# Optimization experiments

Measured on AMD Instinct MI355X. Metric: run time of the kernel, lower is better.

The kernel has to match this reference:

```python
import jax, jax.numpy as jnp
import numpy as np

IN_F = 256
OUT_F = 256
ALPHA = 0.01  # LeakyReLU negative slope
NEG_INF = -1e9


def setup_inputs() -> dict:
    key = jax.random.key(0)
    k_inp, k_adj, k_W, k_a = jax.random.split(key, 4)
    inp = jax.random.normal(k_inp, (8, 2048, IN_F), dtype=jnp.float32)
    adj = jax.random.randint(k_adj, (2048, 2048), 0, 2, dtype=jnp.int32)
    # xavier_uniform with gain=1.414
    gain = 1.414
    lim_W = gain * np.sqrt(6.0 / (IN_F + OUT_F))
    W = jax.random.uniform(k_W, (IN_F, OUT_F), minval=-lim_W, maxval=lim_W, dtype=jnp.float32)
    lim_a = gain * np.sqrt(6.0 / (2 * OUT_F + 1))
    a = jax.random.uniform(k_a, (2 * OUT_F, 1), minval=-lim_a, maxval=lim_a, dtype=jnp.float32)
    return {"inp": inp, "adj": adj, "W": W, "a": a}


def reference(inp, adj, W, a):
    # h: [B, N, F]
    h = jnp.matmul(inp, W)
    # Additive attention decomposed: e_ij = leaky_relu(h_i . a1 + h_j . a2)
    # (mathematically identical to concat([h_i, h_j]) @ a, without the O(N^2 * 2F) intermediate)
    a1 = a[:OUT_F, 0]  # [F]
    a2 = a[OUT_F:, 0]  # [F]
    e_src = jnp.einsum('bnf,f->bn', h, a1)  # [B, N]
    e_dst = jnp.einsum('bnf,f->bn', h, a2)  # [B, N]
    e = jax.nn.leaky_relu(e_src[:, :, None] + e_dst[:, None, :], negative_slope=ALPHA)  # [B, N, N]
    e = jnp.where(adj[None, :, :] == 0, NEG_INF, e)
    attention = jax.nn.softmax(e, axis=-1)
    # dropout is identity in eval mode
    h_prime = jnp.matmul(attention, h)  # [B, N, F]
    return jax.nn.relu(h_prime)  # concat=True path
```

## Files before the change

### kernel.cpp

```cpp
#include <hip/hip_runtime.h>
#include <hip/hip_bf16.h>
#include <stdint.h>

#define N_NODES 2048
#define FDIM 256

typedef short bf16x8 __attribute__((ext_vector_type(8)));
typedef float f32x4 __attribute__((ext_vector_type(4)));
typedef unsigned short u16x4 __attribute__((ext_vector_type(4)));

static __device__ __forceinline__ unsigned short bf16r(float x) {
  __hip_bfloat16 h = __float2bfloat16(x);
  return __builtin_bit_cast(unsigned short, h);
}

static __device__ __forceinline__ void gl_lds16(const void* g, void* l) {
  __builtin_amdgcn_global_load_lds(
      (const __attribute__((address_space(1))) unsigned int*)g,
      (__attribute__((address_space(3))) unsigned int*)l, 16, 0, 0);
}

__global__ __launch_bounds__(256) void k_prep(const float* __restrict__ W, const float* __restrict__ a,
                                              __hip_bfloat16* __restrict__ WT16,
                                              float* __restrict__ wa1, float* __restrict__ wa2) {
  int bid = blockIdx.x, t = threadIdx.x;
  if (bid < 16) {
    __shared__ __hip_bfloat16 T[64][67];
    int k0 = (bid & 3) * 64, f0 = (bid >> 2) * 64;
    int r = t >> 2, c0 = (t & 3) * 16;
    #pragma unroll
    for (int i = 0; i < 4; ++i) {
      f32x4 v = *(const f32x4*)(W + (size_t)(k0 + r) * FDIM + f0 + c0 + i * 4);
      #pragma unroll
      for (int j = 0; j < 4; ++j) T[r][c0 + i * 4 + j] = __float2bfloat16(v[j]);
    }
    __syncthreads();
    int fr = t >> 2, kc = (t & 3) * 16;
    unsigned short buf[16];
    #pragma unroll
    for (int i = 0; i < 16; ++i) buf[i] = __builtin_bit_cast(unsigned short, T[kc + i][fr]);
    uint4* dst = (uint4*)(WT16 + (size_t)(f0 + fr) * FDIM + k0 + kc);
    dst[0] = *(uint4*)&buf[0];
    dst[1] = *(uint4*)&buf[8];
  } else {
    int k = (bid - 16) * 64 + (t >> 2), q = t & 3;
    float s1 = 0.f, s2 = 0.f;
    #pragma unroll
    for (int i = 0; i < 16; ++i) {
      int f = q * 64 + i * 4;
      f32x4 w  = *(const f32x4*)(W + (size_t)k * FDIM + f);
      f32x4 v1 = *(const f32x4*)(a + f);
      f32x4 v2 = *(const f32x4*)(a + FDIM + f);
      #pragma unroll
      for (int j = 0; j < 4; ++j) { s1 += w[j] * v1[j]; s2 += w[j] * v2[j]; }
    }
    s1 += __shfl_xor(s1, 1); s1 += __shfl_xor(s1, 2);
    s2 += __shfl_xor(s2, 1); s2 += __shfl_xor(s2, 2);
    if (q == 0) { wa1[k] = s1; wa2[k] = s2; }
  }
}

__global__ __launch_bounds__(256) void k_h(const float* __restrict__ inp,
                                           const __hip_bfloat16* __restrict__ WT16,
                                           const float* __restrict__ wa1, const float* __restrict__ wa2,
                                           __hip_bfloat16* __restrict__ hT,
                                           float* __restrict__ e_src, float* __restrict__ e_dst) {
  __shared__ char lds_raw[20480];
  __hip_bfloat16* Asm = (__hip_bfloat16*)lds_raw;
  int t = threadIdx.x;
  int r0 = blockIdx.x * 32;
  int b = r0 >> 11, j0 = r0 & (N_NODES - 1);
  {
    int r = t >> 3, q = t & 7, c0 = q * 32;
    const float* ip = inp + (size_t)(r0 + r) * FDIM + c0;
    float s1 = 0.f, s2 = 0.f;
    #pragma unroll
    for (int i = 0; i < 8; ++i) {
      f32x4 v  = *(const f32x4*)(ip + i * 4);
      f32x4 u1 = *(const f32x4*)(wa1 + c0 + i * 4);
      f32x4 u2 = *(const f32x4*)(wa2 + c0 + i * 4);
      u16x4 pk;
      #pragma unroll
      for (int j = 0; j < 4; ++j) {
        s1 += v[j] * u1[j];
        s2 += v[j] * u2[j];
        pk[j] = bf16r(v[j]);
      }
      *(u16x4*)(Asm + r * 264 + c0 + i * 4) = pk;
    }
    s1 += __shfl_xor(s1, 1); s1 += __shfl_xor(s1, 2); s1 += __shfl_xor(s1, 4);
    s2 += __shfl_xor(s2, 1); s2 += __shfl_xor(s2, 2); s2 += __shfl_xor(s2, 4);
    if (q == 0) { e_src[r0 + r] = s1; e_dst[r0 + r] = s2; }
  }
  __syncthreads();

  int lane = t & 63, wv = t >> 6, l15 = lane & 15, lq = lane >> 4;
  int f0 = wv * 64;
  f32x4 acc[2][4];
  #pragma unroll
  for (int mf = 0; mf < 2; ++mf)
    #pragma unroll
    for (int nf = 0; nf < 4; ++nf)
      #pragma unroll
      for (int e = 0; e < 4; ++e) acc[mf][nf][e] = 0.f;

  #pragma unroll
  for (int ks = 0; ks < 8; ++ks) {
    int k0 = ks * 32;
    bf16x8 af[2], bfr[4];
    #pragma unroll
    for (int mf = 0; mf < 2; ++mf)
      af[mf] = *(const bf16x8*)(Asm + (mf * 16 + l15) * 264 + k0 + lq * 8);
    #pragma unroll
    for (int nf = 0; nf < 4; ++nf)
      bfr[nf] = *(const bf16x8*)(WT16 + (size_t)(f0 + nf * 16 + l15) * FDIM + k0 + lq * 8);
    #pragma unroll
    for (int mf = 0; mf < 2; ++mf)
      #pragma unroll
      for (int nf = 0; nf < 4; ++nf)
        acc[mf][nf] = __builtin_amdgcn_mfma_f32_16x16x32_bf16(af[mf], bfr[nf], acc[mf][nf], 0, 0, 0);
  }

  __syncthreads();
  __hip_bfloat16* Tsm = (__hip_bfloat16*)lds_raw;
  #pragma unroll
  for (int mf = 0; mf < 2; ++mf)
    #pragma unroll
    for (int nf = 0; nf < 4; ++nf) {
      u16x4 pk;
      #pragma unroll
      for (int r = 0; r < 4; ++r) pk[r] = bf16r(acc[mf][nf][r]);
      int fl = f0 + nf * 16 + l15;
      int jl = mf * 16 + lq * 4;
      *(u16x4*)(Tsm + fl * 40 + jl) = pk;
    }
  __syncthreads();
  {
    const uint4* src = (const uint4*)(Tsm + t * 40);
    uint4* dst = (uint4*)(hT + ((size_t)b * FDIM + t) * N_NODES + j0);
    dst[0] = src[0]; dst[1] = src[1]; dst[2] = src[2]; dst[3] = src[3];
  }
}

__global__ __launch_bounds__(512) void k_mlp(const int* __restrict__ adj,
                                             const float* __restrict__ e_src,
                                             const float* __restrict__ e_dst,
                                             __hip_bfloat16* __restrict__ P) {
  int t = threadIdx.x, i = blockIdx.x;
  int b = t >> 6, l = t & 63;
  float es = e_src[(b << 11) + i];
  const float* edb = e_dst + ((size_t)b << 11);
  const int* arow = adj + (size_t)i * N_NODES;
  float ev[8][4];
  float mx = -3e38f;
  #pragma unroll
  for (int it = 0; it < 8; ++it) {
    int j0 = it * 256 + l * 4;
    int4 av  = *(const int4*)(arow + j0);
    f32x4 ed = *(const f32x4*)(edb + j0);
    const int* avp = (const int*)&av;
    #pragma unroll
    for (int c = 0; c < 4; ++c) {
      float s = es + ed[c];
      float lr = fmaxf(s, 0.01f * s);
      float e = (avp[c] != 0) ? lr : -1e9f;
      ev[it][c] = e;
      mx = fmaxf(mx, e);
    }
  }
  #pragma unroll
  for (int m = 1; m <= 32; m <<= 1) mx = fmaxf(mx, __shfl_xor(mx, m));
  float sum = 0.f;
  #pragma unroll
  for (int it = 0; it < 8; ++it)
    #pragma unroll
    for (int c = 0; c < 4; ++c) {
      ev[it][c] = __expf(ev[it][c] - mx);
      sum += ev[it][c];
    }
  #pragma unroll
  for (int m = 1; m <= 32; m <<= 1) sum += __shfl_xor(sum, m);
  float il = 1.0f / sum;
  __hip_bfloat16* Pr = P + (((size_t)b << 11) + i) * N_NODES;
  #pragma unroll
  for (int it = 0; it < 8; ++it) {
    int j0 = it * 256 + l * 4;
    u16x4 pk;
    #pragma unroll
    for (int c = 0; c < 4; ++c) pk[c] = bf16r(ev[it][c] * il);
    *(u16x4*)(Pr + j0) = pk;
  }
}

__global__ __launch_bounds__(512) void k_pv(const __hip_bfloat16* __restrict__ P,
                                            const __hip_bfloat16* __restrict__ hT,
                                            float* __restrict__ out) {
  __shared__ __hip_bfloat16 Asm[2 * 64 * 64];
  __shared__ __hip_bfloat16 Bsm[2 * 256 * 64];
  int t = threadIdx.x;
  int b = blockIdx.x & 7;
  int i0 = (blockIdx.x >> 3) * 64;
  int lane = t & 63, wv = t >> 6, l15 = lane & 15, lq = lane >> 4;
  int wm = wv >> 1, wn = wv & 1;
  const __hip_bfloat16* Ab  = P  + ((size_t)(b << 11) + i0) * N_NODES;
  const __hip_bfloat16* hTb = hT + (size_t)b * FDIM * N_NODES;

  int sr = t >> 3, sc = t & 7;
  auto stage = [&](int buf, int js) {
    {
      int cs = sc ^ (sr & 7);
      gl_lds16(Ab + (size_t)sr * N_NODES + js + cs * 8, Asm + buf * 4096 + wv * 512);
    }
    #pragma unroll
    for (int p = 0; p < 4; ++p) {
      int r = p * 64 + sr;
      int cs = sc ^ (r & 7);
      gl_lds16(hTb + (size_t)r * N_NODES + js + cs * 8, Bsm + buf * 16384 + p * 4096 + wv * 512);
    }
  };

  f32x4 acc[8];
  #pragma unroll
  for (int nf = 0; nf < 8; ++nf)
    #pragma unroll
    for (int e = 0; e < 4; ++e) acc[nf][e] = 0.f;

  stage(0, 0);
  __syncthreads();

  int arow = wm * 16 + l15;
  for (int ks = 0; ks < 32; ++ks) {
    int cur = ks & 1;
    if (ks != 31) stage(cur ^ 1, (ks + 1) * 64);
    const __hip_bfloat16* Al = Asm + cur * 4096;
    const __hip_bfloat16* Bl = Bsm + cur * 16384;
    #pragma unroll
    for (int ko = 0; ko < 2; ++ko) {
      int g = ko * 4 + lq;
      bf16x8 af = *(const bf16x8*)(Al + arow * 64 + (g ^ (arow & 7)) * 8);
      #pragma unroll
      for (int nf = 0; nf < 8; ++nf) {
        int br = wn * 128 + nf * 16 + l15;
        bf16x8 bfr = *(const bf16x8*)(Bl + br * 64 + (g ^ (br & 7)) * 8);
        acc[nf] = __builtin_amdgcn_mfma_f32_16x16x32_bf16(af, bfr, acc[nf], 0, 0, 0);
      }
    }
    __syncthreads();
  }

  #pragma unroll
  for (int nf = 0; nf < 8; ++nf)
    #pragma unroll
    for (int r = 0; r < 4; ++r) {
      int row = i0 + wm * 16 + lq * 4 + r;
      int col = wn * 128 + nf * 16 + l15;
      out[((size_t)(b << 11) + row) * FDIM + col] = fmaxf(acc[nf][r], 0.0f);
    }
}

__global__ __launch_bounds__(256) void k_pack(const int* __restrict__ adj, uint32_t* __restrict__ adjp) {
  int t = threadIdx.x;
  int lane = t & 63;
  int i = blockIdx.x * 4 + (t >> 6);
  const int* row = adj + (size_t)i * N_NODES;
  #pragma unroll
  for (int it = 0; it < 32; ++it) {
    int v = row[it * 64 + lane];
    unsigned long long m = __ballot(v != 0);
    if (lane == 0) {
      adjp[i * 64 + it * 2]     = (uint32_t)(m & 0xffffffffull);
      adjp[i * 64 + it * 2 + 1] = (uint32_t)(m >> 32);
    }
  }
}

__global__ __launch_bounds__(256) void k_ml(const uint32_t* __restrict__ adjp,
                                            const float* __restrict__ e_src,
                                            const float* __restrict__ e_dst,
                                            float* __restrict__ mrow, float* __restrict__ ilrow) {
  int t = threadIdx.x;
  int lane = t & 63;
  int r = blockIdx.x * 4 + (t >> 6);
  int b = r >> 11, i = r & (N_NODES - 1);
  float es = e_src[r];
  const float* edb = e_dst + ((size_t)b << 11);
  const uint32_t* arow = adjp + (size_t)i * 64;
  float ev[32];
  float mx = -3e38f;
  #pragma unroll
  for (int it = 0; it < 32; ++it) {
    int j = it * 64 + lane;
    float ed = edb[j];
    uint32_t w = arow[j >> 5];
    float s = es + ed;
    float lr = fmaxf(s, 0.01f * s);
    float e = ((w >> (j & 31)) & 1u) ? lr : -1e9f;
    ev[it] = e;
    mx = fmaxf(mx, e);
  }
  #pragma unroll
  for (int m = 1; m <= 32; m <<= 1) mx = fmaxf(mx, __shfl_xor(mx, m));
  float sum = 0.f;
  #pragma unroll
  for (int it = 0; it < 32; ++it) sum += __expf(ev[it] - mx);
  #pragma unroll
  for (int m = 1; m <= 32; m <<= 1) sum += __shfl_xor(sum, m);
  if (lane == 0) { mrow[r] = mx; ilrow[r] = 1.0f / sum; }
}

__global__ __launch_bounds__(256) void k_pv_f(const __hip_bfloat16* __restrict__ hT,
                                              const uint32_t* __restrict__ adjp,
                                              const float* __restrict__ e_src,
                                              const float* __restrict__ e_dst,
                                              const float* __restrict__ mrow,
                                              const float* __restrict__ ilrow,
                                              float* __restrict__ out) {
  __shared__ __hip_bfloat16 Psm[2][64 * 40];
  int t = threadIdx.x;
  int bb = blockIdx.x & 7;
  int i0 = ((blockIdx.x >> 3) & 31) * 64;
  int fh = (blockIdx.x >> 8) * 128;
  int ip = t >> 2, jq = t & 3;
  int rflat = (bb << 11) + i0 + ip;
  float es = e_src[rflat], mi = mrow[rflat], ili = ilrow[rflat];
  const uint32_t* arow = adjp + (size_t)(i0 + ip) * 64;
  const float* edb = e_dst + ((size_t)bb << 11);
  const __hip_bfloat16* hTb = hT + (size_t)bb * FDIM * N_NODES;
  int lane = t & 63, wv = t >> 6, l15 = lane & 15, lq = lane >> 4;
  int wm = wv >> 1, wn = wv & 1;
  const __hip_bfloat16* bp[4];
  #pragma unroll
  for (int nf = 0; nf < 4; ++nf)
    bp[nf] = hTb + (size_t)(fh + wn * 64 + nf * 16 + l15) * N_NODES + lq * 8;

  auto computeP = [&](int js) -> uint4 {
    uint32_t word = arow[js >> 5] >> (jq * 8);
    f32x4 e0 = *(const f32x4*)(edb + js + jq * 8);
    f32x4 e1 = *(const f32x4*)(edb + js + jq * 8 + 4);
    unsigned short u[8];
    #pragma unroll
    for (int d = 0; d < 8; ++d) {
      float edv = (d < 4) ? e0[d] : e1[d & 3];
      float s = es + edv;
      float lr = fmaxf(s, 0.01f * s);
      float e = ((word >> d) & 1u) ? lr : -1e9f;
      u[d] = bf16r(__expf(e - mi) * ili);
    }
    uint4 r;
    r.x = (uint32_t)u[0] | ((uint32_t)u[1] << 16);
    r.y = (uint32_t)u[2] | ((uint32_t)u[3] << 16);
    r.z = (uint32_t)u[4] | ((uint32_t)u[5] << 16);
    r.w = (uint32_t)u[6] | ((uint32_t)u[7] << 16);
    return r;
  };

  f32x4 acc[2][4];
  #pragma unroll
  for (int mf = 0; mf < 2; ++mf)
    #pragma unroll
    for (int nf = 0; nf < 4; ++nf)
      #pragma unroll
      for (int e = 0; e < 4; ++e) acc[mf][nf][e] = 0.f;

  {
    uint4 p0 = computeP(0);
    *(uint4*)((char*)Psm[0] + ip * 80 + jq * 16) = p0;
  }
  bf16x8 bcur[4];
  #pragma unroll
  for (int nf = 0; nf < 4; ++nf) bcur[nf] = *(const bf16x8*)(bp[nf]);
  __syncthreads();

  int cur = 0;
  for (int js = 0; js < N_NODES; js += 32) {
    bf16x8 bn[4];
    bool more = (js + 32) < N_NODES;
    if (more) {
      #pragma unroll
      for (int nf = 0; nf < 4; ++nf) bn[nf] = *(const bf16x8*)(bp[nf] + js + 32);
      uint4 pn = computeP(js + 32);
      *(uint4*)((char*)Psm[cur ^ 1] + ip * 80 + jq * 16) = pn;
    }
    bf16x8 af[2];
    #pragma unroll
    for (int mf = 0; mf < 2; ++mf)
      af[mf] = *(const bf16x8*)((char*)Psm[cur] + (wm * 32 + mf * 16 + l15) * 80 + lq * 16);
    #pragma unroll
    for (int mf = 0; mf < 2; ++mf)
      #pragma unroll
      for (int nf = 0; nf < 4; ++nf)
        acc[mf][nf] = __builtin_amdgcn_mfma_f32_16x16x32_bf16(af[mf], bcur[nf], acc[mf][nf], 0, 0, 0);
    __syncthreads();
    if (more) {
      #pragma unroll
      for (int nf = 0; nf < 4; ++nf) bcur[nf] = bn[nf];
    }
    cur ^= 1;
  }

  #pragma unroll
  for (int mf = 0; mf < 2; ++mf)
    #pragma unroll
    for (int nf = 0; nf < 4; ++nf)
      #pragma unroll
      for (int r = 0; r < 4; ++r) {
        int row = i0 + wm * 32 + mf * 16 + lq * 4 + r;
        int col = fh + wn * 64 + nf * 16 + l15;
        out[((size_t)bb * N_NODES + row) * FDIM + col] = fmaxf(acc[mf][nf][r], 0.0f);
      }
}

extern "C" void kernel_launch(void* const* d_in, const int* in_sizes, int n_in,
                              void* d_out, int out_size, void* d_ws, size_t ws_size,
                              hipStream_t stream) {
  const float* inp = (const float*)d_in[0];
  const int*   adj = (const int*)d_in[1];
  const float* W   = (const float*)d_in[2];
  const float* a   = (const float*)d_in[3];
  float* out = (float*)d_out;
  char* ws = (char*)d_ws;

  const size_t NEED_BIG = 75761664ull;
  if (ws_size >= NEED_BIG) {
    __hip_bfloat16* P    = (__hip_bfloat16*)ws;
    __hip_bfloat16* hT   = (__hip_bfloat16*)(ws + 67108864);
    float* e_src         = (float*)(ws + 75497472);
    float* e_dst         = (float*)(ws + 75563008);
    __hip_bfloat16* WT16 = (__hip_bfloat16*)(ws + 75628544);
    float* wa1           = (float*)(ws + 75759616);
    float* wa2           = (float*)(ws + 75760640);

    k_prep<<<20, 256, 0, stream>>>(W, a, WT16, wa1, wa2);
    k_h<<<512, 256, 0, stream>>>(inp, WT16, wa1, wa2, hT, e_src, e_dst);
    k_mlp<<<2048, 512, 0, stream>>>(adj, e_src, e_dst, P);
    k_pv<<<256, 512, 0, stream>>>(P, hT, out);
  } else {
    __hip_bfloat16* hT   = (__hip_bfloat16*)ws;
    uint32_t* adjp       = (uint32_t*)(ws + 8388608);
    float* e_src         = (float*)(ws + 8912896);
    float* e_dst         = (float*)(ws + 8978432);
    float* mrow          = (float*)(ws + 9043968);
    float* ilrow         = (float*)(ws + 9109504);
    __hip_bfloat16* WT16 = (__hip_bfloat16*)(ws + 9175040);
    float* wa1           = (float*)(ws + 9306112);
    float* wa2           = (float*)(ws + 9307136);

    k_pack<<<512, 256, 0, stream>>>(adj, adjp);
    k_prep<<<20, 256, 0, stream>>>(W, a, WT16, wa1, wa2);
    k_h<<<512, 256, 0, stream>>>(inp, WT16, wa1, wa2, hT, e_src, e_dst);
    k_ml<<<4096, 256, 0, stream>>>(adjp, e_src, e_dst, mrow, ilrow);
    k_pv_f<<<512, 256, 0, stream>>>(hT, adjp, e_src, e_dst, mrow, ilrow, out);
  }
}
```

Measured before the change: 92.74 us.

## Store P and h in MFMA fragment order and drop LDS staging in PV GEMM

The h-producing and softmax kernels now write their bf16 outputs pre-swizzled into the per-lane MFMA fragment layout. This lets the PV GEMM load fragments directly from global memory with coalesced 16-byte loads and register double-buffering, with no LDS staging and no barriers. The PV wave tiling changes from 4x2 to 2x4 with 2x4 fragment accumulators. The trade-off is that reuse now comes from L2 instead of LDS, and the stores in the softmax kernel are scattered across fragment tiles.

New measurement: 113.8 us, median of 5. +22.7%, slower.

```diff
diff --git a/kernel.cpp b/kernel.cpp
--- a/kernel.cpp
+++ b/kernel.cpp
@@ -12,12 +12,6 @@
 static __device__ __forceinline__ unsigned short bf16r(float x) {
   __hip_bfloat16 h = __float2bfloat16(x);
   return __builtin_bit_cast(unsigned short, h);
-}
-
-static __device__ __forceinline__ void gl_lds16(const void* g, void* l) {
-  __builtin_amdgcn_global_load_lds(
-      (const __attribute__((address_space(1))) unsigned int*)g,
-      (__attribute__((address_space(3))) unsigned int*)l, 16, 0, 0);
 }
 
 __global__ __launch_bounds__(256) void k_prep(const float* __restrict__ W, const float* __restrict__ a,
@@ -58,6 +52,224 @@
     s2 += __shfl_xor(s2, 1); s2 += __shfl_xor(s2, 2);
     if (q == 0) { wa1[k] = s1; wa2[k] = s2; }
   }
+}
+
+__global__ __launch_bounds__(256) void k_h2(const float* __restrict__ inp,
+                                            const __hip_bfloat16* __restrict__ WT16,
+                                            const float* __restrict__ wa1, const float* __restrict__ wa2,
+                                            __hip_bfloat16* __restrict__ Bf,
+                                            float* __restrict__ e_src, float* __restrict__ e_dst) {
+  __shared__ char lds_raw[20480];
+  __hip_bfloat16* Asm = (__hip_bfloat16*)lds_raw;
+  int t = threadIdx.x;
+  int r0 = blockIdx.x * 32;
+  int b = r0 >> 11, j0 = r0 & (N_NODES - 1);
+  {
+    int r = t >> 3, q = t & 7, c0 = q * 32;
+    const float* ip = inp + (size_t)(r0 + r) * FDIM + c0;
+    float s1 = 0.f, s2 = 0.f;
+    #pragma unroll
+    for (int i = 0; i < 8; ++i) {
+      f32x4 v  = *(const f32x4*)(ip + i * 4);
+      f32x4 u1 = *(const f32x4*)(wa1 + c0 + i * 4);
+      f32x4 u2 = *(const f32x4*)(wa2 + c0 + i * 4);
+      u16x4 pk;
+      #pragma unroll
+      for (int j = 0; j < 4; ++j) {
+        s1 += v[j] * u1[j];
+        s2 += v[j] * u2[j];
+        pk[j] = bf16r(v[j]);
+      }
+      *(u16x4*)(Asm + r * 264 + c0 + i * 4) = pk;
+    }
+    s1 += __shfl_xor(s1, 1); s1 += __shfl_xor(s1, 2); s1 += __shfl_xor(s1, 4);
+    s2 += __shfl_xor(s2, 1); s2 += __shfl_xor(s2, 2); s2 += __shfl_xor(s2, 4);
+    if (q == 0) { e_src[r0 + r] = s1; e_dst[r0 + r] = s2; }
+  }
+  __syncthreads();
+
+  int lane = t & 63, wv = t >> 6, l15 = lane & 15, lq = lane >> 4;
+  int f0 = wv * 64;
+  f32x4 acc[2][4];
+  #pragma unroll
+  for (int mf = 0; mf < 2; ++mf)
+    #pragma unroll
+    for (int nf = 0; nf < 4; ++nf)
+      #pragma unroll
+      for (int e = 0; e < 4; ++e) acc[mf][nf][e] = 0.f;
+
+  #pragma unroll
+  for (int ks = 0; ks < 8; ++ks) {
+    int k0 = ks * 32;
+    bf16x8 af[2], bfr[4];
+    #pragma unroll
+    for (int mf = 0; mf < 2; ++mf)
+      af[mf] = *(const bf16x8*)(Asm + (mf * 16 + l15) * 264 + k0 + lq * 8);
+    #pragma unroll
+    for (int nf = 0; nf < 4; ++nf)
+      bfr[nf] = *(const bf16x8*)(WT16 + (size_t)(f0 + nf * 16 + l15) * FDIM + k0 + lq * 8);
+    #pragma unroll
+    for (int mf = 0; mf < 2; ++mf)
+      #pragma unroll
+      for (int nf = 0; nf < 4; ++nf)
+        acc[mf][nf] = __builtin_amdgcn_mfma_f32_16x16x32_bf16(af[mf], bfr[nf], acc[mf][nf], 0, 0, 0);
+  }
+
+  __syncthreads();
+  __hip_bfloat16* Tsm = (__hip_bfloat16*)lds_raw;
+  #pragma unroll
+  for (int mf = 0; mf < 2; ++mf)
+    #pragma unroll
+    for (int nf = 0; nf < 4; ++nf) {
+      u16x4 pk;
+      #pragma unroll
+      for (int r = 0; r < 4; ++r) pk[r] = bf16r(acc[mf][nf][r]);
+      int fl = f0 + nf * 16 + l15;
+      int jl = mf * 16 + lq * 4;
+      *(u16x4*)(Tsm + fl * 40 + jl) = pk;
+    }
+  __syncthreads();
+  {
+    int kt = j0 >> 5;
+    #pragma unroll
+    for (int q = 0; q < 4; ++q) {
+      int ft = (t >> 6) * 4 + q;
+      uint4 v = *(const uint4*)(Tsm + (ft * 16 + l15) * 40 + lq * 8);
+      *(uint4*)(Bf + ((((size_t)b * 16 + ft) * 64 + kt) * 64 + lane) * 8) = v;
+    }
+  }
+}
+
+__global__ __launch_bounds__(512) void k_mlp(const int* __restrict__ adj,
+                                             const float* __restrict__ e_src,
+                                             const float* __restrict__ e_dst,
+                                             __hip_bfloat16* __restrict__ Pf) {
+  int t = threadIdx.x, i = blockIdx.x;
+  int b = t >> 6, l = t & 63;
+  float es = e_src[(b << 11) + i];
+  const float* edb = e_dst + ((size_t)b << 11);
+  const int* arow = adj + (size_t)i * N_NODES;
+  float ev[4][8];
+  float mx = -3e38f;
+  #pragma unroll
+  for (int it = 0; it < 4; ++it) {
+    int j0 = it * 512 + l * 8;
+    int4 a0 = *(const int4*)(arow + j0);
+    int4 a1 = *(const int4*)(arow + j0 + 4);
+    f32x4 e0 = *(const f32x4*)(edb + j0);
+    f32x4 e1 = *(const f32x4*)(edb + j0 + 4);
+    const int* ap0 = (const int*)&a0;
+    const int* ap1 = (const int*)&a1;
+    #pragma unroll
+    for (int c = 0; c < 4; ++c) {
+      float s = es + e0[c];
+      float lr = fmaxf(s, 0.01f * s);
+      float e = (ap0[c] != 0) ? lr : -1e9f;
+      ev[it][c] = e; mx = fmaxf(mx, e);
+    }
+    #pragma unroll
+    for (int c = 0; c < 4; ++c) {
+      float s = es + e1[c];
+      float lr = fmaxf(s, 0.01f * s);
+      float e = (ap1[c] != 0) ? lr : -1e9f;
+      ev[it][c + 4] = e; mx = fmaxf(mx, e);
+    }
+  }
+  #pragma unroll
+  for (int m = 1; m <= 32; m <<= 1) mx = fmaxf(mx, __shfl_xor(mx, m));
+  float sum = 0.f;
+  #pragma unroll
+  for (int it = 0; it < 4; ++it)
+    #pragma unroll
+    for (int c = 0; c < 8; ++c) {
+      ev[it][c] = __expf(ev[it][c] - mx);
+      sum += ev[it][c];
+    }
+  #pragma unroll
+  for (int m = 1; m <= 32; m <<= 1) sum += __shfl_xor(sum, m);
+  float il = 1.0f / sum;
+
+  size_t tile_base = ((size_t)b * 32 + (i >> 6)) * 64 * 4 * 512;
+  int sub = (i >> 4) & 3;
+  int lane_lo = i & 15;
+  #pragma unroll
+  for (int it = 0; it < 4; ++it) {
+    int k0 = it * 16 + (l >> 2);
+    int lanep = ((l & 3) << 4) | lane_lo;
+    unsigned short u[8];
+    #pragma unroll
+    for (int c = 0; c < 8; ++c) u[c] = bf16r(ev[it][c] * il);
+    uint4 v;
+    v.x = (uint32_t)u[0] | ((uint32_t)u[1] << 16);
+    v.y = (uint32_t)u[2] | ((uint32_t)u[3] << 16);
+    v.z = (uint32_t)u[4] | ((uint32_t)u[5] << 16);
+    v.w = (uint32_t)u[6] | ((uint32_t)u[7] << 16);
+    *(uint4*)(Pf + tile_base + ((size_t)(k0 * 4 + sub) * 64 + lanep) * 8) = v;
+  }
+}
+
+struct Frags { bf16x8 a[2]; bf16x8 b[4]; };
+
+__global__ __launch_bounds__(512) void k_pv(const __hip_bfloat16* __restrict__ Pf,
+                                            const __hip_bfloat16* __restrict__ Bf,
+                                            float* __restrict__ out) {
+  int t = threadIdx.x;
+  int b = blockIdx.x & 7;
+  int it = blockIdx.x >> 3;
+  int lane = t & 63, wv = t >> 6, l15 = lane & 15, lq = lane >> 4;
+  int wm = wv >> 2, wn = wv & 3;
+
+  const __hip_bfloat16* Abase = Pf + ((size_t)b * 32 + it) * (64 * 4 * 512) + (size_t)lane * 8;
+  const __hip_bfloat16* Bbase = Bf + (size_t)b * (16 * 64 * 512) + (size_t)lane * 8;
+
+  auto LOAD = [&](int k0) -> Frags {
+    Frags f;
+    #pragma unroll
+    for (int mf = 0; mf < 2; ++mf)
+      f.a[mf] = *(const bf16x8*)(Abase + ((size_t)k0 * 4 + (wm * 2 + mf)) * 512);
+    #pragma unroll
+    for (int nf = 0; nf < 4; ++nf)
+      f.b[nf] = *(const bf16x8*)(Bbase + ((size_t)(wn * 4 + nf) * 64 + k0) * 512);
+    return f;
+  };
+
+  f32x4 acc[2][4];
+  #pragma unroll
+  for (int mf = 0; mf < 2; ++mf)
+    #pragma unroll
+    for (int nf = 0; nf < 4; ++nf)
+      #pragma unroll
+      for (int e = 0; e < 4; ++e) acc[mf][nf][e] = 0.f;
+
+  Frags f0 = LOAD(0);
+  Frags f1 = LOAD(1);
+  for (int k0 = 0; k0 < 64; k0 += 2) {
+    Frags fn0 = LOAD(k0 + 2 < 64 ? k0 + 2 : 0);
+    #pragma unroll
+    for (int mf = 0; mf < 2; ++mf)
+      #pragma unroll
+      for (int nf = 0; nf < 4; ++nf)
+        acc[mf][nf] = __builtin_amdgcn_mfma_f32_16x16x32_bf16(f0.a[mf], f0.b[nf], acc[mf][nf], 0, 0, 0);
+    Frags fn1 = LOAD(k0 + 3 < 64 ? k0 + 3 : 0);
+    #pragma unroll
+    for (int mf = 0; mf < 2; ++mf)
+      #pragma unroll
+      for (int nf = 0; nf < 4; ++nf)
+        acc[mf][nf] = __builtin_amdgcn_mfma_f32_16x16x32_bf16(f1.a[mf], f1.b[nf], acc[mf][nf], 0, 0, 0);
+    f0 = fn0; f1 = fn1;
+  }
+
+  int i0 = it * 64;
+  #pragma unroll
+  for (int mf = 0; mf < 2; ++mf)
+    #pragma unroll
+    for (int nf = 0; nf < 4; ++nf)
+      #pragma unroll
+      for (int r = 0; r < 4; ++r) {
+        int row = i0 + wm * 32 + mf * 16 + lq * 4 + r;
+        int col = wn * 64 + nf * 16 + l15;
+        out[((size_t)(b << 11) + row) * FDIM + col] = fmaxf(acc[mf][nf][r], 0.0f);
+      }
 }
 
 __global__ __launch_bounds__(256) void k_h(const float* __restrict__ inp,
@@ -140,122 +352,6 @@
     uint4* dst = (uint4*)(hT + ((size_t)b * FDIM + t) * N_NODES + j0);
     dst[0] = src[0]; dst[1] = src[1]; dst[2] = src[2]; dst[3] = src[3];
   }
-}
-
-__global__ __launch_bounds__(512) void k_mlp(const int* __restrict__ adj,
-                                             const float* __restrict__ e_src,
-                                             const float* __restrict__ e_dst,
-                                             __hip_bfloat16* __restrict__ P) {
-  int t = threadIdx.x, i = blockIdx.x;
-  int b = t >> 6, l = t & 63;
-  float es = e_src[(b << 11) + i];
-  const float* edb = e_dst + ((size_t)b << 11);
-  const int* arow = adj + (size_t)i * N_NODES;
-  float ev[8][4];
-  float mx = -3e38f;
-  #pragma unroll
-  for (int it = 0; it < 8; ++it) {
-    int j0 = it * 256 + l * 4;
-    int4 av  = *(const int4*)(arow + j0);
-    f32x4 ed = *(const f32x4*)(edb + j0);
-    const int* avp = (const int*)&av;
-    #pragma unroll
-    for (int c = 0; c < 4; ++c) {
-      float s = es + ed[c];
-      float lr = fmaxf(s, 0.01f * s);
-      float e = (avp[c] != 0) ? lr : -1e9f;
-      ev[it][c] = e;
-      mx = fmaxf(mx, e);
-    }
-  }
-  #pragma unroll
-  for (int m = 1; m <= 32; m <<= 1) mx = fmaxf(mx, __shfl_xor(mx, m));
-  float sum = 0.f;
-  #pragma unroll
-  for (int it = 0; it < 8; ++it)
-    #pragma unroll
-    for (int c = 0; c < 4; ++c) {
-      ev[it][c] = __expf(ev[it][c] - mx);
-      sum += ev[it][c];
-    }
-  #pragma unroll
-  for (int m = 1; m <= 32; m <<= 1) sum += __shfl_xor(sum, m);
-  float il = 1.0f / sum;
-  __hip_bfloat16* Pr = P + (((size_t)b << 11) + i) * N_NODES;
-  #pragma unroll
-  for (int it = 0; it < 8; ++it) {
-    int j0 = it * 256 + l * 4;
-    u16x4 pk;
-    #pragma unroll
-    for (int c = 0; c < 4; ++c) pk[c] = bf16r(ev[it][c] * il);
-    *(u16x4*)(Pr + j0) = pk;
-  }
-}
-
-__global__ __launch_bounds__(512) void k_pv(const __hip_bfloat16* __restrict__ P,
-                                            const __hip_bfloat16* __restrict__ hT,
-                                            float* __restrict__ out) {
-  __shared__ __hip_bfloat16 Asm[2 * 64 * 64];
-  __shared__ __hip_bfloat16 Bsm[2 * 256 * 64];
-  int t = threadIdx.x;
-  int b = blockIdx.x & 7;
-  int i0 = (blockIdx.x >> 3) * 64;
-  int lane = t & 63, wv = t >> 6, l15 = lane & 15, lq = lane >> 4;
-  int wm = wv >> 1, wn = wv & 1;
-  const __hip_bfloat16* Ab  = P  + ((size_t)(b << 11) + i0) * N_NODES;
-  const __hip_bfloat16* hTb = hT + (size_t)b * FDIM * N_NODES;
-
-  int sr = t >> 3, sc = t & 7;
-  auto stage = [&](int buf, int js) {
-    {
-      int cs = sc ^ (sr & 7);
-      gl_lds16(Ab + (size_t)sr * N_NODES + js + cs * 8, Asm + buf * 4096 + wv * 512);
-    }
-    #pragma unroll
-    for (int p = 0; p < 4; ++p) {
-      int r = p * 64 + sr;
-      int cs = sc ^ (r & 7);
-      gl_lds16(hTb + (size_t)r * N_NODES + js + cs * 8, Bsm + buf * 16384 + p * 4096 + wv * 512);
-    }
-  };
-
-  f32x4 acc[8];
-  #pragma unroll
-  for (int nf = 0; nf < 8; ++nf)
-    #pragma unroll
-    for (int e = 0; e < 4; ++e) acc[nf][e] = 0.f;
-
-  stage(0, 0);
-  __syncthreads();
-
-  int arow = wm * 16 + l15;
-  for (int ks = 0; ks < 32; ++ks) {
-    int cur = ks & 1;
-    if (ks != 31) stage(cur ^ 1, (ks + 1) * 64);
-    const __hip_bfloat16* Al = Asm + cur * 4096;
-    const __hip_bfloat16* Bl = Bsm + cur * 16384;
-    #pragma unroll
-    for (int ko = 0; ko < 2; ++ko) {
-      int g = ko * 4 + lq;
-      bf16x8 af = *(const bf16x8*)(Al + arow * 64 + (g ^ (arow & 7)) * 8);
-      #pragma unroll
-      for (int nf = 0; nf < 8; ++nf) {
-        int br = wn * 128 + nf * 16 + l15;
-        bf16x8 bfr = *(const bf16x8*)(Bl + br * 64 + (g ^ (br & 7)) * 8);
-        acc[nf] = __builtin_amdgcn_mfma_f32_16x16x32_bf16(af, bfr, acc[nf], 0, 0, 0);
-      }
-    }
-    __syncthreads();
-  }
-
-  #pragma unroll
-  for (int nf = 0; nf < 8; ++nf)
-    #pragma unroll
-    for (int r = 0; r < 4; ++r) {
-      int row = i0 + wm * 16 + lq * 4 + r;
-      int col = wn * 128 + nf * 16 + l15;
-      out[((size_t)(b << 11) + row) * FDIM + col] = fmaxf(acc[nf][r], 0.0f);
-    }
 }
 
 __global__ __launch_bounds__(256) void k_pack(const int* __restrict__ adj, uint32_t* __restrict__ adjp) {
@@ -422,8 +518,8 @@
 
   const size_t NEED_BIG = 75761664ull;
   if (ws_size >= NEED_BIG) {
-    __hip_bfloat16* P    = (__hip_bfloat16*)ws;
-    __hip_bfloat16* hT   = (__hip_bfloat16*)(ws + 67108864);
+    __hip_bfloat16* Pf   = (__hip_bfloat16*)ws;
+    __hip_bfloat16* Bf   = (__hip_bfloat16*)(ws + 67108864);
     float* e_src         = (float*)(ws + 75497472);
     float* e_dst         = (float*)(ws + 75563008);
     __hip_bfloat16* WT16 = (__hip_bfloat16*)(ws + 75628544);
@@ -431,9 +527,9 @@
     float* wa2           = (float*)(ws + 75760640);
 
     k_prep<<<20, 256, 0, stream>>>(W, a, WT16, wa1, wa2);
-    k_h<<<512, 256, 0, stream>>>(inp, WT16, wa1, wa2, hT, e_src, e_dst);
-    k_mlp<<<2048, 512, 0, stream>>>(adj, e_src, e_dst, P);
-    k_pv<<<256, 512, 0, stream>>>(P, hT, out);
+    k_h2<<<512, 256, 0, stream>>>(inp, WT16, wa1, wa2, Bf, e_src, e_dst);
+    k_mlp<<<2048, 512, 0, stream>>>(adj, e_src, e_dst, Pf);
+    k_pv<<<256, 512, 0, stream>>>(Pf, Bf, out);
   } else {
     __hip_bfloat16* hT   = (__hip_bfloat16*)ws;
     uint32_t* adjp       = (uint32_t*)(ws + 8388608);
```
